# Kernel optimization log

Measured on AMD Instinct MI355X. Metric: run time of the kernel, lower is better.

## Reference

```python
import jax, jax.numpy as jnp
import numpy as np
import math

DIM = 1024      # dim == dim_attn (required by value-reshape)
HEAD = 16
KV = 128        # K_v routing slots
HD = DIM // HEAD
N = 50000       # number of nodes


def setup_inputs() -> dict:
    key = jax.random.key(0)
    ks = jax.random.split(key, 8)
    s = lambda fan_in: 1.0 / np.sqrt(fan_in)
    return {
        "x": jax.random.normal(ks[0], (N, DIM), jnp.float32),
        "node_index": jax.random.normal(ks[1], (N, 4), jnp.float32),
        # nn.Linear(dim, dim_attn)
        "Wq": jax.random.normal(ks[2], (DIM, DIM), jnp.float32) * s(DIM),
        "bq": jnp.zeros((DIM,), jnp.float32),
        # nn.Parameter key (K_v, head, head_dim), torch.randn init
        "key_p": jax.random.normal(ks[3], (KV, HEAD, HD), jnp.float32),
        # nn.Linear(dim, dim)
        "Wv": jax.random.normal(ks[4], (DIM, DIM), jnp.float32) * s(DIM),
        "bv": jnp.zeros((DIM,), jnp.float32),
        # gate params, shape (head, 1)
        "alpha": jnp.full((HEAD, 1), math.log(9.0), jnp.float32),
        "beta": jnp.full((HEAD, 1), math.log(0.01), jnp.float32),
        # nn.Linear(4, head*K_v)
        "Wb": jax.random.normal(ks[5], (HEAD * KV, 4), jnp.float32) * s(4),
        "bb": jnp.zeros((HEAD * KV,), jnp.float32),
    }


def _mh_sinkhorn(A, num_iters=3, eps=0.05):
    # A: (N, H, K). Faithful to the per-head torch sinkhorn (Q transposed to
    # (K, N)): row sums are over the node axis, col sums over the slot axis.
    n = A.shape[0]
    k = A.shape[2]
    Q = jnp.exp(A / eps)
    Q = Q / jnp.sum(Q, axis=(0, 2), keepdims=True)          # total-sum norm per head
    for _ in range(num_iters):
        Q = Q / jnp.sum(Q, axis=0, keepdims=True) / k       # rows of Q.T (per slot)
        Q = Q / jnp.sum(Q, axis=2, keepdims=True) / n       # cols of Q.T (per node)
    return Q * n


def reference(x, node_index, Wq, bq, key_p, Wv, bv, alpha, beta, Wb, bb):
    n = x.shape[0]
    q = (x @ Wq.T + bq).reshape(n, HEAD, HD)
    attn = jnp.einsum('nhd,rhd->nhr', q, key_p) / np.float32(np.sqrt(HD))
    bias = (node_index @ Wb.T + bb).reshape(n, HEAD, KV)
    attn = attn + bias                                       # (n, H, K_v)
    xv = (x @ Wv.T + bv).reshape(n, HEAD, HD)
    v = jnp.einsum('nhr,nhd->rhd', jax.nn.sigmoid(attn), xv)  # (K_v, H, D)
    cons = _mh_sinkhorn(jax.nn.softmax(attn, axis=-1))
    v = jnp.einsum('nhr,rhd->nhd', cons, v)
    out = jax.nn.sigmoid(alpha) * xv + jax.nn.sigmoid(beta) * v  # (H,1) broadcasts
    return out.reshape(n, DIM)
```

## Files before the change

kernel.cpp:

```cpp
#include <hip/hip_runtime.h>

#define N_NODES 50000
#define MPAD    50048
#define DIM     1024
#define HEAD    16
#define KV      128
#define HD      64
#define NGRP    98

typedef unsigned short ushort_t;
typedef short short8 __attribute__((ext_vector_type(8)));
typedef float f32x4 __attribute__((ext_vector_type(4)));

__device__ inline unsigned short f2bf(float f){
  union { float f; unsigned u; } v; v.f = f;
  unsigned u = v.u;
  unsigned r = (u + 0x7FFFu + ((u >> 16) & 1u)) >> 16;
  return (unsigned short)r;
}
__device__ inline float bf2f(unsigned short u){
  union { unsigned u; float f; } v; v.u = ((unsigned)u) << 16; return v.f;
}

__device__ inline void gload_lds16(const void* g, void* l){
  __builtin_amdgcn_global_load_lds(
      (const __attribute__((address_space(1))) void*)g,
      (__attribute__((address_space(3))) void*)l, 16, 0, 0);
}

__device__ inline short8 frag64(const ushort_t* lds, int row, int kk, int lane){
  int c  = kk*4 + (lane >> 4);
  int cc = c ^ (row & 7);
  return *(const short8*)(lds + row*64 + cc*8);
}
__device__ inline short8 frag128(const ushort_t* lds, int row, int kk, int lane){
  int c  = kk*4 + (lane >> 4);
  int cc = c ^ (row & 7);
  return *(const short8*)(lds + row*128 + cc*8);
}

__global__ void k_zero(float* p, int n){
  int i = blockIdx.x*256 + threadIdx.x;
  if (i < n) p[i] = 0.f;
}

__global__ void k_prep_x(const float* __restrict__ x, ushort_t* __restrict__ x_bf){
  int idx = blockIdx.x*256 + threadIdx.x;
  int row = idx >> 7, c = idx & 127;
  const float4* s = (const float4*)(x + (size_t)row*1024 + c*8);
  float4 f0 = s[0], f1 = s[1];
  short8 v;
  v[0]=(short)f2bf(f0.x); v[1]=(short)f2bf(f0.y); v[2]=(short)f2bf(f0.z); v[3]=(short)f2bf(f0.w);
  v[4]=(short)f2bf(f1.x); v[5]=(short)f2bf(f1.y); v[6]=(short)f2bf(f1.z); v[7]=(short)f2bf(f1.w);
  int sc = (c & ~7) | ((c ^ row) & 7);
  *(short8*)(x_bf + (size_t)row*1024 + sc*8) = v;
}

__global__ void k_prep_w(const float* __restrict__ Wq, const float* __restrict__ Wv,
                         ushort_t* __restrict__ w_bf){
  int idx = blockIdx.x*256 + threadIdx.x;
  int j = idx >> 10, k = idx & 1023;
  float v = (j < 1024) ? Wq[idx] : Wv[(size_t)(j-1024)*1024 + k];
  int d = k & 63;
  int scol = (k & ~63) | ((((d>>3) ^ (j & 7)) & 7) << 3) | (d & 7);
  w_bf[(size_t)j*1024 + scol] = f2bf(v);
}

__global__ void k_prep_key(const float* __restrict__ key_p, ushort_t* __restrict__ key_bf){
  int idx = blockIdx.x*256 + threadIdx.x;
  int h = idx >> 13, rem = idx & 8191;
  int r = rem >> 6, d = rem & 63;
  float v = key_p[(size_t)(r*HEAD + h)*HD + d];
  int pos = ((((d>>3) ^ (r & 7)) & 7) << 3) | (d & 7);
  key_bf[(size_t)h*8192 + r*64 + pos] = f2bf(v);
}

__global__ void k_vreduce(const float* __restrict__ vp, float* __restrict__ vout){
  int i = blockIdx.x*256 + threadIdx.x;
  float s = 0.f;
  for (int gg = 0; gg < NGRP; ++gg) s += vp[(size_t)gg*131072 + i];
  vout[i] = s;
}

__global__ __launch_bounds__(256) void k_gemm(const ushort_t* __restrict__ x_bf,
    const ushort_t* __restrict__ w_bf, const float* __restrict__ bq,
    const float* __restrict__ bv, ushort_t* __restrict__ q_bf, float* xv_out){
  __shared__ ushort_t a_lds[128*64];
  __shared__ ushort_t b_lds[128*64];
  const int tid = threadIdx.x, lane = tid & 63;
  const int wid = tid >> 6, wr = wid >> 1, wc = wid & 1;
  int b = blockIdx.x;
  int wg = (b & 7)*782 + (b >> 3);
  const int bm0 = (wg >> 4) * 128, bn0 = (wg & 15) * 128;

  f32x4 acc[4][4];
  for (int m=0;m<4;m++) for (int n=0;n<4;n++) acc[m][n] = (f32x4){0.f,0.f,0.f,0.f};

  for (int kt = 0; kt < 16; ++kt){
    const int k0 = kt * 64;
    #pragma unroll
    for (int it = 0; it < 4; ++it){
      int chunk = it*256 + tid;
      int r = chunk >> 3, c = chunk & 7;
      gload_lds16(x_bf + (size_t)(bm0 + r)*1024 + k0 + c*8, a_lds + chunk*8);
    }
    #pragma unroll
    for (int it = 0; it < 4; ++it){
      int chunk = it*256 + tid;
      int r = chunk >> 3, c = chunk & 7;
      gload_lds16(w_bf + (size_t)(bn0 + r)*1024 + k0 + c*8, b_lds + chunk*8);
    }
    __syncthreads();
    #pragma unroll
    for (int kk = 0; kk < 2; ++kk){
      short8 af[4], bfr[4];
      #pragma unroll
      for (int m=0;m<4;m++) af[m]  = frag64(a_lds, wr*64 + m*16 + (lane&15), kk, lane);
      #pragma unroll
      for (int n=0;n<4;n++) bfr[n] = frag64(b_lds, wc*64 + n*16 + (lane&15), kk, lane);
      #pragma unroll
      for (int m=0;m<4;m++)
        #pragma unroll
        for (int n=0;n<4;n++)
          acc[m][n] = __builtin_amdgcn_mfma_f32_16x16x32_bf16(af[m], bfr[n], acc[m][n], 0,0,0);
    }
    __syncthreads();
  }
  #pragma unroll
  for (int n=0;n<4;n++){
    int col = bn0 + wc*64 + n*16 + (lane & 15);
    bool isq = col < 1024;
    float bias = isq ? bq[col] : bv[col - 1024];
    #pragma unroll
    for (int m=0;m<4;m++){
      #pragma unroll
      for (int j=0;j<4;j++){
        int row = bm0 + wr*64 + m*16 + (lane>>4)*4 + j;
        float val = acc[m][n][j] + bias;
        if (isq){
          int d = col & 63;
          int scol = (col & ~63) | ((((d>>3) ^ (row & 7)) & 7) << 3) | (d & 7);
          q_bf[(size_t)row*1024 + scol] = f2bf(val);
        } else if (row < N_NODES){
          xv_out[(size_t)row*1024 + (col - 1024)] = val;
        }
      }
    }
  }
}

template<int PHASE>
__global__ __launch_bounds__(256) void k_attn(
    const ushort_t* __restrict__ q_bf, const ushort_t* __restrict__ key_bf,
    const float* __restrict__ node_index, const float* __restrict__ Wb,
    const float* __restrict__ bb, const float* __restrict__ colsum_in,
    float* __restrict__ colsum_out, const float* __restrict__ v_fin,
    float* __restrict__ v_part, float* xv_out,
    const float* __restrict__ alpha, const float* __restrict__ beta)
{
  constexpr int QB    = (PHASE == 2) ? 1 : 2;
  constexpr int O_Q   = 0;
  constexpr int O_KEY = O_Q + QB*8192;
  constexpr int O_NI  = O_KEY + 16384;
  constexpr int O_WB  = O_NI + QB*1024;
  constexpr int O_RED = O_WB + 2560;
  constexpr int O_COL = O_RED + 2048;
  constexpr int O_W   = O_COL + 512;
  constexpr int O_X1  = O_W + 512;
  constexpr int O_X2  = O_X1 + 16384;

  extern __shared__ char smem[];
  ushort_t* q_lds   = (ushort_t*)(smem + O_Q);
  ushort_t* key_lds = (ushort_t*)(smem + O_KEY);
  float* ni_lds  = (float*)(smem + O_NI);
  float* wb_lds  = (float*)(smem + O_WB);
  float* red_lds = (float*)(smem + O_RED);
  float* col_acc = (float*)(smem + O_COL);
  float* w_lds   = (float*)(smem + O_W);
  ushort_t* sigT     = (ushort_t*)(smem + O_X1);
  ushort_t* xvT      = (ushort_t*)(smem + O_X2);
  ushort_t* vT       = (ushort_t*)(smem + O_X1);
  ushort_t* cons_lds = (ushort_t*)(smem + O_X2);
  float*    out_lds  = (float*)(smem + O_X2);

  const int tid = threadIdx.x, lane = tid & 63, wid = tid >> 6;
  const int h    = blockIdx.x & 15;
  const int g    = blockIdx.x >> 4;
  const int base = g * 512;
  int NT = (MPAD - base) >> 6; if (NT > 8) NT = 8;

  #pragma unroll
  for (int it = 0; it < 4; ++it){
    int chunk = it*256 + tid;
    gload_lds16(key_bf + (size_t)h*8192 + chunk*8, key_lds + chunk*8);
  }
  #pragma unroll
  for (int it = 0; it < 2; ++it){
    int chunk = it*256 + tid;
    int r = chunk >> 3, c = chunk & 7;
    gload_lds16(q_bf + (size_t)(base + r)*1024 + h*64 + c*8, q_lds + chunk*8);
  }
  { int r = tid >> 2, c = tid & 3;
    ni_lds[tid] = (base + r < N_NODES) ? node_index[(size_t)(base + r)*4 + c] : 0.f; }
  if (tid < 128){
    #pragma unroll
    for (int c=0;c<4;c++) wb_lds[tid*5+c] = Wb[(size_t)(h*128 + tid)*4 + c];
    wb_lds[tid*5+4] = bb[h*128 + tid];
    if (PHASE >= 1) w_lds[tid] = 1.f / (128.f * colsum_in[h*128 + tid]);
    if (PHASE <= 1) col_acc[tid] = 0.f;
  }
  if constexpr (PHASE == 2){
    int r = tid >> 1, dh = (tid & 1)*32;
    #pragma unroll
    for (int i=0;i<32;i++){
      int d = dh + i;
      vT[d*128 + ((r>>3) ^ (d&7))*8 + (r&7)] = f2bf(v_fin[((size_t)r*16 + h)*64 + d]);
    }
  }
  float xvr[16], xvn[16];
  if constexpr (PHASE == 0){
    int d = tid & 63, q4 = tid >> 6;
    #pragma unroll
    for (int i=0;i<16;i++){
      int row = base + q4*16 + i;
      xvr[i] = (row < N_NODES) ? xv_out[(size_t)row*1024 + h*64 + d] : 0.f;
    }
  }
  f32x4 vac[2][4];
  if constexpr (PHASE == 0)
    for (int m=0;m<2;m++) for (int n=0;n<4;n++) vac[m][n] = (f32x4){0.f,0.f,0.f,0.f};

  __syncthreads();

  for (int t = 0; t < NT; ++t){
    const int i0  = base + t*64;
    const int cur = t & 1;
    const ushort_t* qb  = q_lds  + ((QB==2) ? cur*4096 : 0);
    const float*    nib = ni_lds + ((QB==2) ? cur*256  : 0);
    float ni_next = 0.f;

    if constexpr (QB == 2){
      if (t+1 < NT){
        int i1 = i0 + 64;
        #pragma unroll
        for (int it = 0; it < 2; ++it){
          int chunk = it*256 + tid;
          int r = chunk >> 3, c = chunk & 7;
          gload_lds16(q_bf + (size_t)(i1 + r)*1024 + h*64 + c*8,
                      q_lds + (cur^1)*4096 + chunk*8);
        }
        int r = tid >> 2, c = tid & 3;
        ni_next = (i0 + 64 + r < N_NODES) ? node_index[(size_t)(i0+64+r)*4 + c] : 0.f;
      }
    } else {
      if (t+1 < NT){
        int r = tid >> 2, c = tid & 3;
        ni_next = (i0 + 64 + r < N_NODES) ? node_index[(size_t)(i0+64+r)*4 + c] : 0.f;
      }
    }
    if constexpr (PHASE == 0){
      if (t+1 < NT){
        int d = tid & 63, q4 = tid >> 6;
        #pragma unroll
        for (int i=0;i<16;i++){
          int row = i0 + 64 + q4*16 + i;
          xvn[i] = (row < N_NODES) ? xv_out[(size_t)row*1024 + h*64 + d] : 0.f;
        }
      }
    }

    f32x4 acc[2][4];
    for (int m=0;m<2;m++) for (int n=0;n<4;n++) acc[m][n] = (f32x4){0.f,0.f,0.f,0.f};
    #pragma unroll
    for (int kk = 0; kk < 2; ++kk){
      short8 kf[2];
      #pragma unroll
      for (int m=0;m<2;m++) kf[m] = frag64(key_lds, wid*32 + m*16 + (lane&15), kk, lane);
      #pragma unroll
      for (int n=0;n<4;n++){
        short8 qf = frag64(qb, n*16 + (lane&15), kk, lane);
        #pragma unroll
        for (int m=0;m<2;m++)
          acc[m][n] = __builtin_amdgcn_mfma_f32_16x16x32_bf16(kf[m], qf, acc[m][n], 0,0,0);
      }
    }

    float nif[4][4];
    #pragma unroll
    for (int n=0;n<4;n++){
      int nn = n*16 + (lane&15);
      #pragma unroll
      for (int c=0;c<4;c++) nif[n][c] = nib[nn*4+c];
    }
    float a[2][4][4];
    #pragma unroll
    for (int m=0;m<2;m++){
      #pragma unroll
      for (int j=0;j<4;j++){
        int r = wid*32 + m*16 + (lane>>4)*4 + j;
        float w0 = wb_lds[r*5+0], w1 = wb_lds[r*5+1];
        float w2 = wb_lds[r*5+2], w3 = wb_lds[r*5+3], w4 = wb_lds[r*5+4];
        #pragma unroll
        for (int n=0;n<4;n++){
          float b = w4 + w0*nif[n][0] + w1*nif[n][1] + w2*nif[n][2] + w3*nif[n][3];
          a[m][n][j] = acc[m][n][j]*0.125f + b;
        }
      }
    }

    float vmask[4];
    #pragma unroll
    for (int n=0;n<4;n++) vmask[n] = (i0 + n*16 + (lane&15) < N_NODES) ? 1.f : 0.f;

    if constexpr (PHASE == 0){
      #pragma unroll
      for (int m=0;m<2;m++) for (int n=0;n<4;n++) for (int j=0;j<4;j++){
        int r  = wid*32 + m*16 + (lane>>4)*4 + j;
        int nn = n*16 + (lane&15);
        float sg = vmask[n] / (1.f + __expf(-a[m][n][j]));
        sigT[r*64 + ((((nn>>3) ^ (r&7)) & 7) << 3) + (nn&7)] = f2bf(sg);
      }
      { int d = tid & 63, q4 = tid >> 6;
        #pragma unroll
        for (int i=0;i<16;i++){
          int nn = q4*16 + i;
          xvT[d*64 + ((((nn>>3) ^ (d&7)) & 7) << 3) + (nn&7)] = f2bf(xvr[i]);
        }
      }
    }

    float pm[4];
    #pragma unroll
    for (int n=0;n<4;n++){
      float m0 = a[0][n][0];
      #pragma unroll
      for (int m=0;m<2;m++) for (int j=0;j<4;j++) m0 = fmaxf(m0, a[m][n][j]);
      m0 = fmaxf(m0, __shfl_xor(m0, 16));
      m0 = fmaxf(m0, __shfl_xor(m0, 32));
      pm[n] = m0;
    }
    if (lane < 16){
      #pragma unroll
      for (int n=0;n<4;n++) red_lds[wid*64 + n*16 + lane] = pm[n];
    }
    __syncthreads();

    if constexpr (QB == 1){
      if (t+1 < NT){
        int i1 = i0 + 64;
        #pragma unroll
        for (int it = 0; it < 2; ++it){
          int chunk = it*256 + tid;
          int r = chunk >> 3, c = chunk & 7;
          gload_lds16(q_bf + (size_t)(i1 + r)*1024 + h*64 + c*8, q_lds + chunk*8);
        }
        ni_lds[tid] = ni_next;
      }
    }

    float mnn[4], snn[4];
    #pragma unroll
    for (int n=0;n<4;n++){
      int nn = n*16 + (lane&15);
      float m0 = red_lds[nn];
      m0 = fmaxf(m0, red_lds[64+nn]); m0 = fmaxf(m0, red_lds[128+nn]); m0 = fmaxf(m0, red_lds[192+nn]);
      mnn[n] = m0;
    }
    #pragma unroll
    for (int n=0;n<4;n++){
      float s = 0.f;
      #pragma unroll
      for (int m=0;m<2;m++) for (int j=0;j<4;j++){
        float e = __expf(a[m][n][j] - mnn[n]);
        a[m][n][j] = e; s += e;
      }
      s += __shfl_xor(s, 16); s += __shfl_xor(s, 32);
      snn[n] = s;
    }
    if (lane < 16){
      #pragma unroll
      for (int n=0;n<4;n++) red_lds[256 + wid*64 + n*16 + lane] = snn[n];
    }

    if constexpr (PHASE == 0){
      #pragma unroll
      for (int kk=0;kk<2;kk++){
        short8 sa[2];
        #pragma unroll
        for (int m=0;m<2;m++) sa[m] = frag64(sigT, wid*32 + m*16 + (lane&15), kk, lane);
        #pragma unroll
        for (int n=0;n<4;n++){
          short8 xf = frag64(xvT, n*16 + (lane&15), kk, lane);
          #pragma unroll
          for (int m=0;m<2;m++)
            vac[m][n] = __builtin_amdgcn_mfma_f32_16x16x32_bf16(sa[m], xf, vac[m][n], 0,0,0);
        }
      }
    }
    __syncthreads();

    #pragma unroll
    for (int n=0;n<4;n++){
      int nn = n*16 + (lane&15);
      snn[n] = red_lds[256+nn] + red_lds[256+64+nn] + red_lds[256+128+nn] + red_lds[256+192+nn];
    }
    #pragma unroll
    for (int n=0;n<4;n++){
      float inv = 20.f / snn[n];
      #pragma unroll
      for (int m=0;m<2;m++) for (int j=0;j<4;j++)
        a[m][n][j] = __expf(a[m][n][j] * inv);
    }

    float uval[4];
    if constexpr (PHASE >= 1){
      #pragma unroll
      for (int n=0;n<4;n++){
        float s = 0.f;
        #pragma unroll
        for (int m=0;m<2;m++){
          #pragma unroll
          for (int j=0;j<4;j++){
            int r = wid*32 + m*16 + (lane>>4)*4 + j;
            s += a[m][n][j] * w_lds[r];
          }
        }
        s += __shfl_xor(s, 16); s += __shfl_xor(s, 32);
        uval[n] = s;
      }
      if (lane < 16){
        #pragma unroll
        for (int n=0;n<4;n++) red_lds[wid*64 + n*16 + lane] = uval[n];
      }
      __syncthreads();
      #pragma unroll
      for (int n=0;n<4;n++){
        int nn = n*16 + (lane&15);
        float s = red_lds[nn] + red_lds[64+nn] + red_lds[128+nn] + red_lds[192+nn];
        uval[n] = 1.f / (50000.f * s);
      }
    }

    if constexpr (PHASE <= 1){
      float cs[2][4];
      #pragma unroll
      for (int m=0;m<2;m++){
        #pragma unroll
        for (int j=0;j<4;j++){
          float s = 0.f;
          #pragma unroll
          for (int n=0;n<4;n++){
            float tv = a[m][n][j] * vmask[n];
            if (PHASE == 1) tv *= uval[n];
            s += tv;
          }
          s += __shfl_xor(s, 1); s += __shfl_xor(s, 2);
          s += __shfl_xor(s, 4); s += __shfl_xor(s, 8);
          cs[m][j] = s;
        }
      }
      if ((lane & 15) == 0){
        #pragma unroll
        for (int m=0;m<2;m++) for (int j=0;j<4;j++){
          int r = wid*32 + m*16 + (lane>>4)*4 + j;
          col_acc[r] += cs[m][j];
        }
      }
    }

    if constexpr (PHASE == 2){
      #pragma unroll
      for (int m=0;m<2;m++) for (int n=0;n<4;n++) for (int j=0;j<4;j++){
        int r  = wid*32 + m*16 + (lane>>4)*4 + j;
        int nn = n*16 + (lane&15);
        float cv = 50000.f * uval[n] * a[m][n][j] * w_lds[r];
        cons_lds[nn*128 + ((r>>3) ^ (nn&7))*8 + (r&7)] = f2bf(cv);
      }
      __syncthreads();
      f32x4 oac[4];
      for (int n=0;n<4;n++) oac[n] = (f32x4){0.f,0.f,0.f,0.f};
      #pragma unroll
      for (int kk=0;kk<4;kk++){
        short8 va = frag128(vT, wid*16 + (lane&15), kk, lane);
        #pragma unroll
        for (int n=0;n<4;n++){
          short8 cf = frag128(cons_lds, n*16 + (lane&15), kk, lane);
          oac[n] = __builtin_amdgcn_mfma_f32_16x16x32_bf16(va, cf, oac[n], 0,0,0);
        }
      }
      __syncthreads();
      #pragma unroll
      for (int n=0;n<4;n++) for (int j=0;j<4;j++){
        int d  = wid*16 + (lane>>4)*4 + j;
        int nn = n*16 + (lane&15);
        out_lds[nn*68 + d] = oac[n][j];
      }
      __syncthreads();
      float sa = 1.f/(1.f + __expf(-alpha[h]));
      float sb = 1.f/(1.f + __expf(-beta[h]));
      int nn = tid >> 2, d0 = (tid & 3)*16;
      if (i0 + nn < N_NODES){
        #pragma unroll
        for (int gq=0; gq<4; ++gq){
          float4 vf = *(const float4*)(out_lds + nn*68 + d0 + gq*4);
          float4 xf = *(const float4*)(xv_out + (size_t)(i0+nn)*1024 + h*64 + d0 + gq*4);
          float4 o;
          o.x = sa*xf.x + sb*vf.x;
          o.y = sa*xf.y + sb*vf.y;
          o.z = sa*xf.z + sb*vf.z;
          o.w = sa*xf.w + sb*vf.w;
          *(float4*)(xv_out + (size_t)(i0+nn)*1024 + h*64 + d0 + gq*4) = o;
        }
      }
    } else {
      if (t+1 < NT && QB == 2) ni_lds[(cur^1)*256 + tid] = ni_next;
      if constexpr (PHASE == 0){
        if (t+1 < NT){
          #pragma unroll
          for (int i=0;i<16;i++) xvr[i] = xvn[i];
        }
      }
      __syncthreads();
    }
  }

  if constexpr (PHASE == 0){
    float* vdst = v_part + (size_t)g*131072;
    #pragma unroll
    for (int m=0;m<2;m++) for (int n=0;n<4;n++) for (int j=0;j<4;j++){
      int r = wid*32 + m*16 + (lane>>4)*4 + j;
      int d = n*16 + (lane&15);
      vdst[((size_t)r*16 + h)*64 + d] = vac[m][n][j];
    }
  }
  if constexpr (PHASE <= 1){
    if (tid < 128) atomicAdd(&colsum_out[h*128 + tid], col_acc[tid]);
  }
}

extern "C" void kernel_launch(void* const* d_in, const int* in_sizes, int n_in,
                              void* d_out, int out_size, void* d_ws, size_t ws_size,
                              hipStream_t stream){
  const float* x     = (const float*)d_in[0];
  const float* ni    = (const float*)d_in[1];
  const float* Wq    = (const float*)d_in[2];
  const float* bq    = (const float*)d_in[3];
  const float* keyp  = (const float*)d_in[4];
  const float* Wv    = (const float*)d_in[5];
  const float* bv    = (const float*)d_in[6];
  const float* alpha = (const float*)d_in[7];
  const float* beta  = (const float*)d_in[8];
  const float* Wb    = (const float*)d_in[9];
  const float* bb    = (const float*)d_in[10];
  float* out = (float*)d_out;

  char* ws = (char*)d_ws;
  ushort_t* x_bf   = (ushort_t*)(ws);
  float*    v_part = (float*)(ws);
  ushort_t* q_bf   = (ushort_t*)(ws + 102498304);
  ushort_t* w_bf   = (ushort_t*)(ws + 204996608);
  ushort_t* key_bf = (ushort_t*)(ws + 209190912);
  float*    v_fin  = (float*)(ws + 209453056);
  float*    cs     = (float*)(ws + 209977344);

  k_zero<<<dim3(24), 256, 0, stream>>>(cs, 6144);
  k_prep_x<<<dim3(25000), 256, 0, stream>>>(x, x_bf);
  k_prep_w<<<dim3(2048*1024/256), 256, 0, stream>>>(Wq, Wv, w_bf);
  k_prep_key<<<dim3(HEAD*KV*HD/256), 256, 0, stream>>>(keyp, key_bf);
  k_gemm<<<dim3(6256), 256, 0, stream>>>(x_bf, w_bf, bq, bv, q_bf, out);

  dim3 ag(NGRP*16);
  k_attn<0><<<ag, 256, 65024, stream>>>(q_bf, key_bf, ni, Wb, bb, nullptr,  cs,      v_fin, v_part, out, alpha, beta);
  k_vreduce<<<dim3(512), 256, 0, stream>>>(v_part, v_fin);
  k_attn<1><<<ag, 256, 40448, stream>>>(q_bf, key_bf, ni, Wb, bb, cs,       cs+2048, v_fin, v_part, out, alpha, beta);
  k_attn<1><<<ag, 256, 40448, stream>>>(q_bf, key_bf, ni, Wb, bb, cs+2048,  cs+4096, v_fin, v_part, out, alpha, beta);
  k_attn<2><<<ag, 256, 65024, stream>>>(q_bf, key_bf, ni, Wb, bb, cs+4096,  nullptr, v_fin, v_part, out, alpha, beta);
}
```

Baseline: 1.042 ms.

## Enlarge GEMM tile to 256x256 with double-buffered async LDS pipeline

Rewrites the fused Q/V projection GEMM to use 256x256 output tiles with 512 threads, each wave computing 128x64. LDS loads are double-buffered and issued asynchronously two stages ahead, with vmcnt waits. The aim is better operand reuse and overlap of global loads with MFMA work. In exchange the kernel uses 128KB of dynamic LDS, which limits occupancy, and the row padding grows, so the workspace offsets shift and the extra pad rows must be zeroed.

```diff
diff --git a/kernel.cpp b/kernel.cpp
--- a/kernel.cpp
+++ b/kernel.cpp
@@ -1,7 +1,7 @@
 #include <hip/hip_runtime.h>
 
 #define N_NODES 50000
-#define MPAD    50048
+#define MPAD    50176
 #define DIM     1024
 #define HEAD    16
 #define KV      128
@@ -82,60 +82,83 @@
   vout[i] = s;
 }
 
-__global__ __launch_bounds__(256) void k_gemm(const ushort_t* __restrict__ x_bf,
+__global__ __launch_bounds__(512) void k_gemm(const ushort_t* __restrict__ x_bf,
     const ushort_t* __restrict__ w_bf, const float* __restrict__ bq,
     const float* __restrict__ bv, ushort_t* __restrict__ q_bf, float* xv_out){
-  __shared__ ushort_t a_lds[128*64];
-  __shared__ ushort_t b_lds[128*64];
+  extern __shared__ char gsm[];
+  ushort_t* As = (ushort_t*)gsm;
+  ushort_t* Bs = (ushort_t*)(gsm + 65536);
   const int tid = threadIdx.x, lane = tid & 63;
-  const int wid = tid >> 6, wr = wid >> 1, wc = wid & 1;
+  const int wid = tid >> 6, wr = wid >> 2, wc = wid & 3;
   int b = blockIdx.x;
-  int wg = (b & 7)*782 + (b >> 3);
-  const int bm0 = (wg >> 4) * 128, bn0 = (wg & 15) * 128;
-
-  f32x4 acc[4][4];
-  for (int m=0;m<4;m++) for (int n=0;n<4;n++) acc[m][n] = (f32x4){0.f,0.f,0.f,0.f};
+  int wg = (b & 7)*196 + (b >> 3);
+  const int bm0 = (wg >> 3) * 256, bn0 = (wg & 7) * 256;
+
+  f32x4 acc[8][4];
+  #pragma unroll
+  for (int m=0;m<8;m++)
+    #pragma unroll
+    for (int n=0;n<4;n++) acc[m][n] = (f32x4){0.f,0.f,0.f,0.f};
+
+  const ushort_t* asrc = x_bf + (size_t)bm0*1024;
+  const ushort_t* bsrc = w_bf + (size_t)bn0*1024;
+
+#define STAGE(kt, bi)                                                    \
+  { _Pragma("unroll")                                                    \
+    for (int it=0; it<4; ++it){                                          \
+      int chunk = it*512 + tid;                                          \
+      int r = chunk >> 3, c = chunk & 7;                                 \
+      gload_lds16(asrc + (size_t)r*1024 + (kt)*64 + c*8,                 \
+                  As + (bi)*16384 + chunk*8);                            \
+    }                                                                    \
+    _Pragma("unroll")                                                    \
+    for (int it=0; it<4; ++it){                                          \
+      int chunk = it*512 + tid;                                          \
+      int r = chunk >> 3, c = chunk & 7;                                 \
+      gload_lds16(bsrc + (size_t)r*1024 + (kt)*64 + c*8,                 \
+                  Bs + (bi)*16384 + chunk*8);                            \
+    }                                                                    \
+  }
+
+  STAGE(0, 0);
+  STAGE(1, 1);
 
   for (int kt = 0; kt < 16; ++kt){
-    const int k0 = kt * 64;
-    #pragma unroll
-    for (int it = 0; it < 4; ++it){
-      int chunk = it*256 + tid;
-      int r = chunk >> 3, c = chunk & 7;
-      gload_lds16(x_bf + (size_t)(bm0 + r)*1024 + k0 + c*8, a_lds + chunk*8);
-    }
-    #pragma unroll
-    for (int it = 0; it < 4; ++it){
-      int chunk = it*256 + tid;
-      int r = chunk >> 3, c = chunk & 7;
-      gload_lds16(w_bf + (size_t)(bn0 + r)*1024 + k0 + c*8, b_lds + chunk*8);
-    }
-    __syncthreads();
-    #pragma unroll
-    for (int kk = 0; kk < 2; ++kk){
-      short8 af[4], bfr[4];
-      #pragma unroll
-      for (int m=0;m<4;m++) af[m]  = frag64(a_lds, wr*64 + m*16 + (lane&15), kk, lane);
-      #pragma unroll
-      for (int n=0;n<4;n++) bfr[n] = frag64(b_lds, wc*64 + n*16 + (lane&15), kk, lane);
-      #pragma unroll
-      for (int m=0;m<4;m++)
+    const int cur = kt & 1;
+    if (kt == 15) { asm volatile("s_waitcnt vmcnt(0)" ::: "memory"); }
+    else          { asm volatile("s_waitcnt vmcnt(8)" ::: "memory"); }
+    __builtin_amdgcn_s_barrier();
+
+    const ushort_t* ab  = As + cur*16384;
+    const ushort_t* bb_ = Bs + cur*16384;
+    #pragma unroll
+    for (int kk=0;kk<2;kk++){
+      short8 bfr[4];
+      #pragma unroll
+      for (int n=0;n<4;n++) bfr[n] = frag64(bb_, wc*64 + n*16 + (lane&15), kk, lane);
+      #pragma unroll
+      for (int m=0;m<8;m++){
+        short8 af = frag64(ab, wr*128 + m*16 + (lane&15), kk, lane);
         #pragma unroll
         for (int n=0;n<4;n++)
-          acc[m][n] = __builtin_amdgcn_mfma_f32_16x16x32_bf16(af[m], bfr[n], acc[m][n], 0,0,0);
-    }
-    __syncthreads();
-  }
+          acc[m][n] = __builtin_amdgcn_mfma_f32_16x16x32_bf16(af, bfr[n], acc[m][n], 0,0,0);
+      }
+    }
+    __builtin_amdgcn_s_barrier();
+    if (kt + 2 < 16) STAGE(kt+2, cur);
+  }
+#undef STAGE
+
+  const bool isq = bn0 < 1024;
   #pragma unroll
   for (int n=0;n<4;n++){
     int col = bn0 + wc*64 + n*16 + (lane & 15);
-    bool isq = col < 1024;
     float bias = isq ? bq[col] : bv[col - 1024];
     #pragma unroll
-    for (int m=0;m<4;m++){
+    for (int m=0;m<8;m++){
       #pragma unroll
       for (int j=0;j<4;j++){
-        int row = bm0 + wr*64 + m*16 + (lane>>4)*4 + j;
+        int row = bm0 + wr*128 + m*16 + (lane>>4)*4 + j;
         float val = acc[m][n][j] + bias;
         if (isq){
           int d = col & 63;
@@ -557,17 +580,21 @@
   char* ws = (char*)d_ws;
   ushort_t* x_bf   = (ushort_t*)(ws);
   float*    v_part = (float*)(ws);
-  ushort_t* q_bf   = (ushort_t*)(ws + 102498304);
-  ushort_t* w_bf   = (ushort_t*)(ws + 204996608);
-  ushort_t* key_bf = (ushort_t*)(ws + 209190912);
-  float*    v_fin  = (float*)(ws + 209453056);
-  float*    cs     = (float*)(ws + 209977344);
+  ushort_t* q_bf   = (ushort_t*)(ws + 102760448);
+  ushort_t* w_bf   = (ushort_t*)(ws + 205520896);
+  ushort_t* key_bf = (ushort_t*)(ws + 209715200);
+  float*    v_fin  = (float*)(ws + 209977344);
+  float*    cs     = (float*)(ws + 210501632);
+
+  (void)hipFuncSetAttribute((const void*)k_gemm,
+      hipFuncAttributeMaxDynamicSharedMemorySize, 131072);
 
   k_zero<<<dim3(24), 256, 0, stream>>>(cs, 6144);
+  k_zero<<<dim3(352), 256, 0, stream>>>((float*)(x_bf + (size_t)N_NODES*1024), 90112);
   k_prep_x<<<dim3(25000), 256, 0, stream>>>(x, x_bf);
   k_prep_w<<<dim3(2048*1024/256), 256, 0, stream>>>(Wq, Wv, w_bf);
   k_prep_key<<<dim3(HEAD*KV*HD/256), 256, 0, stream>>>(keyp, key_bf);
-  k_gemm<<<dim3(6256), 256, 0, stream>>>(x_bf, w_bf, bq, bv, q_bf, out);
+  k_gemm<<<dim3(1568), 512, 131072, stream>>>(x_bf, w_bf, bq, bv, q_bf, out);
 
   dim3 ag(NGRP*16);
   k_attn<0><<<ag, 256, 65024, stream>>>(q_bf, key_bf, ni, Wb, bb, nullptr,  cs,      v_fin, v_part, out, alpha, beta);
```

New measurement: 943.9 us. 1.1x faster.
